# Kernel tuning notes

Hardware: AMD Instinct MI355X
Metric: run time of the kernel (lower is better)

The kernel has to match this reference:

```python
import jax, jax.numpy as jnp
import numpy as np

N = 128000      # total nodes
B = 128         # graphs, 1000 nodes each
L = 4           # max_levels
S_MAX = 1000    # max cluster size (<= PositionalEncoding max_len)
H = 128         # hidden dim (all conv output dims equal)
IN_DIM = 128
OUT_DIM = 1
E = 1024000
TEMP = 0.1


def layer_norm(x, g, b, eps=1e-5):
    mu = jnp.mean(x, axis=-1, keepdims=True)
    v = jnp.mean((x - mu) ** 2, axis=-1, keepdims=True)
    return (x - mu) * jax.lax.rsqrt(v + eps) * g + b


def transformer_conv(x, src, dst, Wq, bq, Wk, bk, Wv, bv, Ws, bs):
    # PyG TransformerConv, heads=1: softmax over in-edges of each dst node
    q = x @ Wq + bq
    k = x @ Wk + bk
    v = x @ Wv + bv
    logits = jnp.sum(q[dst] * k[src], axis=-1) / jnp.sqrt(jnp.float32(q.shape[-1]))
    m = jax.ops.segment_max(logits, dst, num_segments=N)
    e = jnp.exp(logits - m[dst])
    s = jax.ops.segment_sum(e, dst, num_segments=N)
    alpha = e / s[dst]
    agg = jax.ops.segment_sum(alpha[:, None] * v[src], dst, num_segments=N)
    return agg + x @ Ws + bs  # root_weight skip connection


def pos_encoding(S, d):
    pos = jnp.arange(S, dtype=jnp.float32)[:, None]
    div = jnp.exp(jnp.arange(0, d, 2, dtype=jnp.float32) * (-jnp.log(10000.0) / d))
    pe = jnp.zeros((S, d), jnp.float32)
    pe = pe.at[:, 0::2].set(jnp.sin(pos * div))
    pe = pe.at[:, 1::2].set(jnp.cos(pos * div))
    return pe


def gru(xseq, Wih, Whh, bih, bhh):
    # xseq: [G, S, H] -> outputs [G, S, H]; torch GRU gate math
    G = xseq.shape[0]
    def step(h, x_t):
        gi = x_t @ Wih.T + bih
        gh = h @ Whh.T + bhh
        ir, iz, inn = jnp.split(gi, 3, axis=-1)
        hr, hz, hn = jnp.split(gh, 3, axis=-1)
        r = jax.nn.sigmoid(ir + hr)
        z = jax.nn.sigmoid(iz + hz)
        n = jnp.tanh(inn + r * hn)
        h_new = (1.0 - z) * n + z * h
        return h_new, h_new
    h0 = jnp.zeros((G, Whh.shape[1]), xseq.dtype)
    _, outs = jax.lax.scan(step, h0, jnp.swapaxes(xseq, 0, 1))
    return jnp.swapaxes(outs, 0, 1)


def _forward(x, tree_edge_index, call_sequences, batch,
             conv_Wq, conv_bq, conv_Wk, conv_bk, conv_Wv, conv_bv, conv_Ws, conv_bs,
             ln_g, ln_b, centers, proj_W, proj_b,
             gru_Wih, gru_Whh, gru_bih, gru_bhh, seqln_g, seqln_b,
             lin1_W, lin1_b, lin2_W, lin2_b):
    src, dst = tree_edge_index[0], tree_edge_index[1]
    h = x
    for i in range(3):  # conv1/bn1, conv2/bn2, conv4/bn4
        h = transformer_conv(h, src, dst, conv_Wq[i], conv_bq[i], conv_Wk[i],
                             conv_bk[i], conv_Wv[i], conv_bv[i], conv_Ws[i], conv_bs[i])
        h = jax.nn.relu(layer_norm(h, ln_g[i], ln_b[i]))

    # HierarchicalClassifier: cosine-sim soft assignment + center variance loss
    xn = h / jnp.maximum(jnp.linalg.norm(h, axis=-1, keepdims=True), 1e-8)
    cn = centers / jnp.maximum(jnp.linalg.norm(centers, axis=-1, keepdims=True), 1e-8)
    assign = jax.nn.softmax((xn @ cn.T) / TEMP, axis=-1)
    level_ids = jnp.argmax(assign, axis=1).astype(jnp.int32)
    iu0, iu1 = np.triu_indices(L, k=1)
    dvec = jnp.linalg.norm(centers[iu0] - centers[iu1], axis=-1)
    distance = -jnp.var(dvec, ddof=1)  # torch.var is unbiased

    # ragged gather + pad: group nodes by (graph, cluster), sort by call order
    G = B * L
    group = batch * L + level_ids                       # [N]
    order = jnp.argsort(group * N + call_sequences)     # sort by group, then call
    g_sorted = group[order]
    counts = jax.ops.segment_sum(jnp.ones((N,), jnp.int32), group, num_segments=G)
    starts = jnp.cumsum(counts) - counts
    pos = jnp.arange(N, dtype=jnp.int32) - starts[g_sorted]
    seq = jnp.zeros((G, S_MAX, H), h.dtype).at[g_sorted, pos].set(h[order])

    # SequentialRNN: proj -> pos-enc -> GRU -> LayerNorm -> ReLU (mask unused)
    sin = seq @ proj_W + proj_b + pos_encoding(S_MAX, H)[None]
    outs = gru(sin, gru_Wih, gru_Whh, gru_bih, gru_bhh)
    outs = jax.nn.relu(layer_norm(outs, seqln_g, seqln_b))

    # scatter valid positions back; singleton clusters keep raw features
    node_out = jnp.zeros_like(h).at[order].set(outs[g_sorted, pos])
    singleton = (counts[group] == 1)
    gout = jnp.where(singleton[:, None], h, node_out)

    y = jax.nn.gelu(gout @ lin1_W + lin1_b, approximate=False)
    y = jax.nn.sigmoid(y @ lin2_W + lin2_b)
    return y, distance


def setup_inputs():
    key = jax.random.key(0)
    ks = jax.random.split(key, 16)
    p = lambda k, s: jax.random.normal(k, s, jnp.float32) * 0.02
    return {
        "x": jax.random.normal(ks[0], (N, IN_DIM), jnp.float32),
        "tree_edge_index": jax.random.randint(ks[1], (2, E), 0, N, dtype=jnp.int32),
        "call_sequences": jax.random.permutation(ks[2], N).astype(jnp.int32),
        "batch": (jnp.arange(N, dtype=jnp.int32) * B) // N,  # 1000 nodes per graph
        "conv_Wq": p(ks[3], (3, H, H)), "conv_bq": jnp.zeros((3, H), jnp.float32),
        "conv_Wk": p(ks[4], (3, H, H)), "conv_bk": jnp.zeros((3, H), jnp.float32),
        "conv_Wv": p(ks[5], (3, H, H)), "conv_bv": jnp.zeros((3, H), jnp.float32),
        "conv_Ws": p(ks[6], (3, H, H)), "conv_bs": jnp.zeros((3, H), jnp.float32),
        "ln_g": jnp.ones((3, H), jnp.float32), "ln_b": jnp.zeros((3, H), jnp.float32),
        "centers": jax.random.normal(ks[7], (L, H), jnp.float32),
        "proj_W": p(ks[8], (H, H)), "proj_b": jnp.zeros((H,), jnp.float32),
        "gru_Wih": p(ks[9], (3 * H, H)), "gru_Whh": p(ks[10], (3 * H, H)),
        "gru_bih": jnp.zeros((3 * H,), jnp.float32), "gru_bhh": jnp.zeros((3 * H,), jnp.float32),
        "seqln_g": jnp.ones((H,), jnp.float32), "seqln_b": jnp.zeros((H,), jnp.float32),
        "lin1_W": p(ks[11], (H, 8)), "lin1_b": jnp.zeros((8,), jnp.float32),
        "lin2_W": p(ks[12], (8, OUT_DIM)), "lin2_b": jnp.zeros((OUT_DIM,), jnp.float32),
    }


def reference(x, tree_edge_index, call_sequences, batch,
              conv_Wq, conv_bq, conv_Wk, conv_bk, conv_Wv, conv_bv, conv_Ws, conv_bs,
              ln_g, ln_b, centers, proj_W, proj_b,
              gru_Wih, gru_Whh, gru_bih, gru_bhh, seqln_g, seqln_b,
              lin1_W, lin1_b, lin2_W, lin2_b):
    return _forward(x, tree_edge_index, call_sequences, batch,
                    conv_Wq, conv_bq, conv_Wk, conv_bk, conv_Wv, conv_bv, conv_Ws, conv_bs,
                    ln_g, ln_b, centers, proj_W, proj_b,
                    gru_Wih, gru_Whh, gru_bih, gru_bhh, seqln_g, seqln_b,
                    lin1_W, lin1_b, lin2_W, lin2_b)
```

## Files before the change

### kernel.cpp

```cpp
#include <hip/hip_runtime.h>

#define NN 128000
#define EE 1024000
#define HH 128
#define GG 512
#define SMAX 1000
#define NCHUNK 500

typedef unsigned int u32;
typedef unsigned short u16;

constexpr size_t NH     = (size_t)NN*HH;
constexpr size_t F_H    = 0;
constexpr size_t F_A    = NH;
constexpr size_t F_B    = 2*NH;
constexpr size_t F_NODE = F_A + (size_t)NN*192;
constexpr size_t F_QB   = 3*NH;
constexpr size_t F_CN   = F_QB  + NN;
constexpr size_t F_WKT  = F_CN  + 512;
constexpr size_t F_CW   = F_WKT + 3*16384;
constexpr size_t F_PEW  = F_CW  + 128*384;
constexpr size_t F_PEB  = F_PEW + 1000*384;
constexpr size_t F_END  = F_PEB + 1000*128;

constexpr size_t I_ROWP = 0;
constexpr size_t I_CUR  = I_ROWP + NN + 8;
constexpr size_t I_COL  = I_CUR  + NN;
constexpr size_t I_GRP  = I_COL  + EE;
constexpr size_t I_INV  = I_GRP  + NN;
constexpr size_t I_POS  = I_INV  + NN;
constexpr size_t I_GN   = I_POS  + NN;
constexpr size_t I_CNT  = I_GN   + (size_t)GG*SMAX;
constexpr size_t I_CH   = I_CNT  + GG;
constexpr size_t I_BS   = I_CH   + (size_t)NCHUNK*GG;
constexpr size_t I_WT   = I_BS   + 512;
constexpr size_t I_END  = I_WT   + 64*384;

constexpr size_t WS_NEEDED = F_END*4 + I_END*4;

__device__ inline float wredf(float v){
  #pragma unroll
  for (int o = 32; o; o >>= 1) v += __shfl_xor(v, o);
  return v;
}
__device__ inline u32 bf16rne(float f){
  u32 u = __float_as_uint(f);
  return (u + 0x7fffu + ((u >> 16) & 1u)) >> 16;
}
__device__ inline float bf2f(u16 u){
  return __uint_as_float(((u32)u) << 16);
}
__device__ inline float frcp(float x){
#if __has_builtin(__builtin_amdgcn_rcpf)
  return __builtin_amdgcn_rcpf(x);
#else
  return 1.f / x;
#endif
}

typedef _Float16 h2_t __attribute__((ext_vector_type(2)));
__device__ inline float dot2f(u32 w, u32 h, float acc){
#if __has_builtin(__builtin_amdgcn_fdot2)
  return __builtin_amdgcn_fdot2(__builtin_bit_cast(h2_t, w),
                                __builtin_bit_cast(h2_t, h), acc, false);
#else
  float r;
  asm("v_dot2_f32_f16 %0, %1, %2, %3" : "=v"(r) : "v"(w), "v"(h), "v"(acc));
  return r;
#endif
}
#define PIN4(v) asm volatile("" : "+v"((v).x), "+v"((v).y), "+v"((v).z), "+v"((v).w))

__global__ void k_sentinel(float* __restrict__ out, int n, float val){
  int i = blockIdx.x * 256 + threadIdx.x;
  if (i < n) out[i] = val;
}

__global__ void k_zero(int* __restrict__ p){
  p[blockIdx.x * 256 + threadIdx.x] = 0;
}
__global__ void k_hist(const int* __restrict__ dst, int* __restrict__ deg){
  int e = blockIdx.x * 256 + threadIdx.x;
  atomicAdd(&deg[dst[e]], 1);
}
__global__ void k_s1(const int* __restrict__ deg, int* __restrict__ bsum){
  __shared__ int red[256];
  int t = threadIdx.x;
  red[t] = deg[blockIdx.x * 256 + t];
  __syncthreads();
  for (int s = 128; s; s >>= 1){ if (t < s) red[t] += red[t + s]; __syncthreads(); }
  if (!t) bsum[blockIdx.x] = red[0];
}
__global__ void k_s2(int* __restrict__ bsum){
  __shared__ int arr[512];
  int t = threadIdx.x;
  int v0 = (t < NCHUNK) ? bsum[t] : 0;
  arr[t] = v0; __syncthreads();
  for (int off = 1; off < 512; off <<= 1){
    int v = (t >= off) ? arr[t - off] : 0;
    __syncthreads();
    arr[t] += v;
    __syncthreads();
  }
  if (t < NCHUNK) bsum[t] = arr[t] - v0;
}
__global__ void k_s3(const int* __restrict__ bsum, int* __restrict__ row_ptr,
                     int* __restrict__ cursor){
  __shared__ int arr[256];
  int t = threadIdx.x;
  int i = blockIdx.x * 256 + t;
  int v0 = cursor[i];
  arr[t] = v0; __syncthreads();
  for (int off = 1; off < 256; off <<= 1){
    int v = (t >= off) ? arr[t - off] : 0;
    __syncthreads();
    arr[t] += v;
    __syncthreads();
  }
  int exc = arr[t] - v0 + bsum[blockIdx.x];
  row_ptr[i] = exc;
  cursor[i]  = exc;
  if (i == 0) row_ptr[NN] = EE;
}
__global__ void k_scatter(const int* __restrict__ src, const int* __restrict__ dst,
                          int* __restrict__ cursor, int* __restrict__ col){
  int e = blockIdx.x * 256 + threadIdx.x;
  int idx = atomicAdd(&cursor[dst[e]], 1);
  col[idx] = src[e];
}

__global__ void k_setup(const float* __restrict__ centers, float* __restrict__ cn,
                        float* __restrict__ dist_out){
  __shared__ float red[128];
  int t = threadIdx.x;
  for (int l = 0; l < 4; ++l){
    float v = centers[l*128 + t];
    red[t] = v * v; __syncthreads();
    for (int s = 64; s; s >>= 1){ if (t < s) red[t] += red[t + s]; __syncthreads(); }
    float nrm = sqrtf(red[0]);
    __syncthreads();
    cn[l*128 + t] = v / fmaxf(nrm, 1e-8f);
  }
  const int iu0[6] = {0,0,0,1,1,2}, iu1[6] = {1,2,3,2,3,3};
  __shared__ float dv[6];
  for (int p = 0; p < 6; ++p){
    float d = centers[iu0[p]*128 + t] - centers[iu1[p]*128 + t];
    red[t] = d * d; __syncthreads();
    for (int s = 64; s; s >>= 1){ if (t < s) red[t] += red[t + s]; __syncthreads(); }
    if (!t) dv[p] = sqrtf(red[0]);
    __syncthreads();
  }
  if (!t){
    float mean = 0.f;
    for (int p = 0; p < 6; ++p) mean += dv[p];
    mean /= 6.f;
    float var = 0.f;
    for (int p = 0; p < 6; ++p){ float d = dv[p] - mean; var += d * d; }
    var /= 5.f;
    dist_out[0] = -var;
  }
}

__global__ void k_pe(const float* __restrict__ projb, float* __restrict__ peb){
  int p = blockIdx.x, t = threadIdx.x;
  float ex  = (float)(t >> 1) * (-2.0f * 9.210340371976184f / 128.0f);
  float ang = (float)p * expf(ex);
  float v = (t & 1) ? cosf(ang) : sinf(ang);
  peb[p*128 + t] = v + projb[t];
}
__global__ void k_pew(const float* __restrict__ peb, const float* __restrict__ Wih,
                      const float* __restrict__ bih, float* __restrict__ pew){
  int p = blockIdx.x;
  int j = blockIdx.y * 128 + threadIdx.x;
  const float* pb = peb + p*128;
  const float* wr = Wih + (size_t)j*128;
  float acc = bih[j];
  #pragma unroll 4
  for (int m = 0; m < 128; ++m) acc += pb[m] * wr[m];
  pew[(size_t)p*384 + j] = acc;
}
__global__ void k_combw(const float* __restrict__ projW, const float* __restrict__ Wih,
                        float* __restrict__ cw){
  int kk = blockIdx.x;
  int j  = blockIdx.y * 128 + threadIdx.x;
  const float* pr = projW + (size_t)kk*128;
  const float* wr = Wih + (size_t)j*128;
  float acc = 0.f;
  #pragma unroll 4
  for (int m = 0; m < 128; ++m) acc += pr[m] * wr[m];
  cw[(size_t)kk*384 + j] = acc;
}
__global__ void k_tr(const float* __restrict__ Wk, float* __restrict__ wkt){
  int kk = blockIdx.x, l = blockIdx.y, c = threadIdx.x;
  wkt[(size_t)l*16384 + kk*128 + c] = Wk[(size_t)l*16384 + c*128 + kk];
}
__global__ void k_packwhh16(const float* __restrict__ Whh, u32* __restrict__ wt){
  int kp = blockIdx.x;
  int j  = blockIdx.y * 128 + threadIdx.x;
  _Float16 a = (_Float16)Whh[(size_t)j*128 + 2*kp];
  _Float16 b = (_Float16)Whh[(size_t)j*128 + 2*kp + 1];
  u32 lo = (u32)__builtin_bit_cast(u16, a);
  u32 hi = (u32)__builtin_bit_cast(u16, b);
  wt[(size_t)j*64 + kp] = (hi << 16) | lo;
}

__global__ __launch_bounds__(256, 2) void k_gemm(
    const float* __restrict__ X, const float* __restrict__ W, int ldw,
    const float* __restrict__ X2, const float* __restrict__ W2,
    const float* __restrict__ bias, const float* __restrict__ pew,
    const int* __restrict__ pos, float* __restrict__ out,
    u16* __restrict__ outb, int ldo){
  __shared__ __align__(16) float Wl[64*132];
  __shared__ __align__(16) float Xl[64*132];
  int tid = threadIdx.x;
  int rb = blockIdx.x * 128;
  int cb = blockIdx.y * 128;
  int rg = tid >> 4;
  int cg = tid & 15;
  int kxor = (cg >> 2) & 3;
  float acc[8][8];
  #pragma unroll
  for (int a = 0; a < 8; ++a)
    #pragma unroll
    for (int b = 0; b < 8; ++b) acc[a][b] = 0.f;
  int nhalf = X2 ? 4 : 2;
  for (int half = 0; half < nhalf; ++half){
    const float* Xs = (half < 2) ? X : X2;
    const float* Ws = (half < 2) ? W : W2;
    int ldws = (half < 2) ? ldw : 128;
    int hk = half & 1;
    __syncthreads();
    #pragma unroll
    for (int it = 0; it < 8; ++it){
      int idx = it*256 + tid;
      int kk = idx >> 5, c4 = idx & 31;
      *(float4*)&Wl[kk*132 + c4*4] =
          *(const float4*)&Ws[(size_t)(hk*64 + kk)*ldws + cb + c4*4];
    }
    #pragma unroll
    for (int it = 0; it < 8; ++it){
      int idx = it*256 + tid;
      int r = idx >> 4, c4 = idx & 15;
      float4 xv = *(const float4*)&Xs[(size_t)(rb + r)*128 + hk*64 + c4*4];
      Xl[(c4*4+0)*132 + r] = xv.x;
      Xl[(c4*4+1)*132 + r] = xv.y;
      Xl[(c4*4+2)*132 + r] = xv.z;
      Xl[(c4*4+3)*132 + r] = xv.w;
    }
    __syncthreads();
    #pragma unroll 2
    for (int kk = 0; kk < 64; ++kk){
      int kx = kk ^ kxor;
      float4 wa = *(const float4*)&Wl[kx*132 + cg*8];
      float4 wb = *(const float4*)&Wl[kx*132 + cg*8 + 4];
      float4 xa = *(const float4*)&Xl[kx*132 + rg*8];
      float4 xb = *(const float4*)&Xl[kx*132 + rg*8 + 4];
      float xs[8] = {xa.x, xa.y, xa.z, xa.w, xb.x, xb.y, xb.z, xb.w};
      float ws[8] = {wa.x, wa.y, wa.z, wa.w, wb.x, wb.y, wb.z, wb.w};
      #pragma unroll
      for (int rr = 0; rr < 8; ++rr)
        #pragma unroll
        for (int j = 0; j < 8; ++j) acc[rr][j] += xs[rr] * ws[j];
    }
  }
  #pragma unroll
  for (int rr = 0; rr < 8; ++rr){
    int r = rb + rg*8 + rr;
    float bv[8];
    if (pos){
      const float* pw = pew + (size_t)pos[r]*384 + cb + cg*8;
      #pragma unroll
      for (int j = 0; j < 8; ++j) bv[j] = pw[j];
    } else if (bias){
      #pragma unroll
      for (int j = 0; j < 8; ++j) bv[j] = bias[cb + cg*8 + j];
    } else {
      #pragma unroll
      for (int j = 0; j < 8; ++j) bv[j] = 0.f;
    }
    if (outb){
      u16 ob[8];
      #pragma unroll
      for (int j = 0; j < 8; ++j) ob[j] = (u16)bf16rne(acc[rr][j] + bv[j]);
      *(uint4*)(outb + (size_t)r*ldo + cb + cg*8) = *(const uint4*)ob;
    } else {
      float ov[8];
      #pragma unroll
      for (int j = 0; j < 8; ++j) ov[j] = acc[rr][j] + bv[j];
      float* op = out + (size_t)r*ldo + cb + cg*8;
      *(float4*)op       = *(const float4*)&ov[0];
      *(float4*)(op + 4) = *(const float4*)&ov[4];
    }
  }
}

__global__ __launch_bounds__(256) void k_rowdot(
    const float* __restrict__ q, const float* __restrict__ bk,
    float* __restrict__ qb){
  int d = blockIdx.x * 4 + (threadIdx.x >> 6);
  int lane = threadIdx.x & 63;
  float2 qv = *(const float2*)&q[(size_t)d*128 + 2*lane];
  float2 bv = *(const float2*)&bk[2*lane];
  float p = wredf(qv.x * bv.x + qv.y * bv.y);
  if (lane == 0) qb[d] = p;
}

__global__ __launch_bounds__(256) void k_edge(
    const float* __restrict__ qt, const float* __restrict__ qb,
    const float* __restrict__ xsrc, const int* __restrict__ row_ptr,
    const int* __restrict__ col, float* __restrict__ xagg){
  int d = blockIdx.x * 4 + (threadIdx.x >> 6);
  int lane = threadIdx.x & 63;
  int e0 = row_ptr[d], e1 = row_ptr[d+1];
  if (e0 == e1){
    *(float2*)&xagg[(size_t)d*128 + 2*lane] = make_float2(0.f, 0.f);
    return;
  }
  float2 qv = *(const float2*)&qt[(size_t)d*128 + 2*lane];
  float qbd = qb[d];
  float ssum = 0.f, a0 = 0.f, a1 = 0.f;
  for (int e = e0; e < e1; ++e){
    int s = col[e];
    float2 xv = *(const float2*)&xsrc[(size_t)s*128 + 2*lane];
    float p = wredf(qv.x * xv.x + qv.y * xv.y);
    float el = __expf((p + qbd) * 0.08838834764831845f);
    ssum += el;
    a0 += el * xv.x;
    a1 += el * xv.y;
  }
  float inv = 1.f / ssum;
  *(float2*)&xagg[(size_t)d*128 + 2*lane] = make_float2(a0 * inv, a1 * inv);
}

__global__ __launch_bounds__(256) void k_lnrelu(
    const float* __restrict__ in, const float* __restrict__ g,
    const float* __restrict__ b, const float* __restrict__ bvv,
    const int* __restrict__ rowp, float* __restrict__ outp){
  int node = blockIdx.x * 4 + (threadIdx.x >> 6);
  int lane = threadIdx.x & 63;
  float x0 = in[(size_t)node*128 + 2*lane], x1 = in[(size_t)node*128 + 2*lane + 1];
  if (bvv && rowp[node+1] > rowp[node]){
    x0 += bvv[2*lane];
    x1 += bvv[2*lane + 1];
  }
  float s = wredf(x0 + x1);
  float qq = wredf(x0*x0 + x1*x1);
  float mu = s * 0.0078125f;
  float var = qq * 0.0078125f - mu*mu;
  float rstd = rsqrtf(var + 1e-5f);
  float y0 = (x0 - mu)*rstd*g[2*lane]   + b[2*lane];
  float y1 = (x1 - mu)*rstd*g[2*lane+1] + b[2*lane+1];
  outp[(size_t)node*128 + 2*lane]     = fmaxf(y0, 0.f);
  outp[(size_t)node*128 + 2*lane + 1] = fmaxf(y1, 0.f);
}

__global__ __launch_bounds__(256) void k_postln(
    u16* __restrict__ no, const float* __restrict__ g, const float* __restrict__ b){
  int node = blockIdx.x * 4 + (threadIdx.x >> 6);
  int lane = threadIdx.x & 63;
  float x0 = bf2f(no[(size_t)node*128 + 2*lane]);
  float x1 = bf2f(no[(size_t)node*128 + 2*lane + 1]);
  float s = wredf(x0 + x1);
  float qq = wredf(x0*x0 + x1*x1);
  float mu = s * 0.0078125f;
  float var = qq * 0.0078125f - mu*mu;
  float rstd = rsqrtf(var + 1e-5f);
  float y0 = (x0 - mu)*rstd*g[2*lane]   + b[2*lane];
  float y1 = (x1 - mu)*rstd*g[2*lane+1] + b[2*lane+1];
  no[(size_t)node*128 + 2*lane]     = (u16)bf16rne(fmaxf(y0, 0.f));
  no[(size_t)node*128 + 2*lane + 1] = (u16)bf16rne(fmaxf(y1, 0.f));
}

__global__ __launch_bounds__(256) void k_classify(
    const float* __restrict__ h, const float* __restrict__ cn,
    const int* __restrict__ batch, const int* __restrict__ callsq,
    int* __restrict__ grp, int* __restrict__ inv){
  int node = blockIdx.x * 4 + (threadIdx.x >> 6);
  int lane = threadIdx.x & 63;
  float h0 = h[(size_t)node*128 + 2*lane], h1 = h[(size_t)node*128 + 2*lane + 1];
  float p0 = h0*cn[      2*lane] + h1*cn[      2*lane+1];
  float p1 = h0*cn[128 + 2*lane] + h1*cn[128 + 2*lane+1];
  float p2 = h0*cn[256 + 2*lane] + h1*cn[256 + 2*lane+1];
  float p3 = h0*cn[384 + 2*lane] + h1*cn[384 + 2*lane+1];
  p0 = wredf(p0); p1 = wredf(p1); p2 = wredf(p2); p3 = wredf(p3);
  if (lane == 0){
    float best = p0; int bi = 0;
    if (p1 > best){ best = p1; bi = 1; }
    if (p2 > best){ best = p2; bi = 2; }
    if (p3 > best){ best = p3; bi = 3; }
    grp[node] = batch[node]*4 + bi;
    inv[callsq[node]] = node;
  }
}

__global__ __launch_bounds__(256) void k_g1(const int* __restrict__ inv,
                                            const int* __restrict__ grp,
                                            int* __restrict__ ch){
  __shared__ int hist[GG];
  int c = blockIdx.x, t = threadIdx.x;
  hist[t] = 0; hist[t + 256] = 0;
  __syncthreads();
  int g = grp[inv[c*256 + t]];
  atomicAdd(&hist[g], 1);
  __syncthreads();
  ch[c*GG + t] = hist[t];
  ch[c*GG + 256 + t] = hist[256 + t];
}
__global__ void k_g2(int* __restrict__ ch, int* __restrict__ cnt){
  __shared__ int arr[512];
  int g = blockIdx.x, t = threadIdx.x;
  int v0 = (t < NCHUNK) ? ch[(size_t)t*GG + g] : 0;
  arr[t] = v0; __syncthreads();
  for (int off = 1; off < 512; off <<= 1){
    int v = (t >= off) ? arr[t - off] : 0;
    __syncthreads();
    arr[t] += v;
    __syncthreads();
  }
  if (t < NCHUNK) ch[(size_t)t*GG + g] = arr[t] - v0;
  if (t == 511) cnt[g] = arr[511];
}
__global__ __launch_bounds__(256) void k_g3(
    const int* __restrict__ inv, const int* __restrict__ grp,
    const int* __restrict__ ch, int* __restrict__ pos, int* __restrict__ gn){
  __shared__ int hist[GG];
  int c = blockIdx.x, t = threadIdx.x;
  hist[t] = 0; hist[t + 256] = 0;
  __syncthreads();
  int node = inv[c*256 + t];
  int g = grp[node];
  int lane = t & 63, w = t >> 6;
  int before = 0, total = 0;
  for (int j = 0; j < 64; ++j){
    int gj = __shfl(g, j);
    if (gj == g){ total++; if (j < lane) before++; }
  }
  int base = 0;
  for (int wv = 0; wv < 4; ++wv){
    if (w == wv){
      base = hist[g];
      if (before == total - 1) hist[g] = base + total;
    }
    __syncthreads();
  }
  int p = ch[c*GG + g] + base + before;
  pos[node] = p;
  gn[(size_t)g*SMAX + p] = node;
}

__global__ __launch_bounds__(256)
__attribute__((amdgpu_waves_per_eu(2, 2)))
void k_gru(
    const u16* __restrict__ gi, const u32* __restrict__ wt,
    const float* __restrict__ bhh, const int* __restrict__ gn,
    const int* __restrict__ cnt, u16* __restrict__ node_out){
  __shared__ __align__(16) u16 hb16[2][128];
  int t = threadIdx.x;
  int j = t >> 1;
  int kh = t & 1;
  int g = blockIdx.x;
  int my = cnt[g];
  if (my <= 1) return;
  uint4 wr_[8], wz_[8], wn_[8];
  {
    const uint4* wt4 = (const uint4*)wt;
    size_t b0 = (size_t)(0*128 + j)*16 + kh*8;
    size_t b1 = (size_t)(1*128 + j)*16 + kh*8;
    size_t b2 = (size_t)(2*128 + j)*16 + kh*8;
    #pragma unroll
    for (int s = 0; s < 8; ++s){
      wr_[s] = wt4[b0 + s];
      wz_[s] = wt4[b1 + s];
      wn_[s] = wt4[b2 + s];
    }
    #pragma unroll
    for (int s = 0; s < 8; ++s){
      PIN4(wr_[s]); PIN4(wz_[s]); PIN4(wn_[s]);
    }
  }
  if (t < 128) hb16[0][t] = 0;
  float br = bhh[j], bz = bhh[128 + j], bn = bhh[256 + j];
  const int* gnr = gn + (size_t)g*SMAX;
  float hprev = 0.f;
  int nA = gnr[0];
  int nB = gnr[min(1, my - 1)];
  int nC = gnr[min(2, my - 1)];
  const u16* gA = gi + (size_t)nA*384;
  const u16* gB = gi + (size_t)nB*384;
  const u16* gC = gi + (size_t)nC*384;
  float axr = bf2f(gA[j]), axz = bf2f(gA[128 + j]), axn = bf2f(gA[256 + j]);
  float bxr = bf2f(gB[j]), bxz = bf2f(gB[128 + j]), bxn = bf2f(gB[256 + j]);
  float cxr = bf2f(gC[j]), cxz = bf2f(gC[128 + j]), cxn = bf2f(gC[256 + j]);
  __syncthreads();
  for (int p = 0; p < my; ++p){
    int cur = p & 1, nxt = cur ^ 1;
    float xr = axr, xz = axz, xn = axn;
    int node = nA;
    axr = bxr; axz = bxz; axn = bxn; nA = nB;
    bxr = cxr; bxz = cxz; bxn = cxn; nB = nC;
    nC = gnr[min(p + 3, my - 1)];
    const u16* gN = gi + (size_t)nC*384;
    cxr = bf2f(gN[j]); cxz = bf2f(gN[128 + j]); cxn = bf2f(gN[256 + j]);
    const uint4* HB = (const uint4*)&hb16[cur][0];
    uint4 hh[8];
    #pragma unroll
    for (int s = 0; s < 8; ++s) hh[s] = HB[kh*8 + s];
    float ar = 0.f, az = 0.f, an = 0.f;
    #pragma unroll
    for (int s = 0; s < 8; ++s){
      ar = dot2f(wr_[s].x, hh[s].x, ar); az = dot2f(wz_[s].x, hh[s].x, az); an = dot2f(wn_[s].x, hh[s].x, an);
      ar = dot2f(wr_[s].y, hh[s].y, ar); az = dot2f(wz_[s].y, hh[s].y, az); an = dot2f(wn_[s].y, hh[s].y, an);
      ar = dot2f(wr_[s].z, hh[s].z, ar); az = dot2f(wz_[s].z, hh[s].z, az); an = dot2f(wn_[s].z, hh[s].z, an);
      ar = dot2f(wr_[s].w, hh[s].w, ar); az = dot2f(wz_[s].w, hh[s].w, az); an = dot2f(wn_[s].w, hh[s].w, an);
    }
    ar += __shfl_xor(ar, 1); az += __shfl_xor(az, 1); an += __shfl_xor(an, 1);
    ar += br; az += bz; an += bn;
    float er = __expf(-(xr + ar));
    float r  = frcp(1.f + er);
    float ez = __expf(-(xz + az));
    float z  = frcp(1.f + ez);
    float y  = xn + r * an;
    float e2 = __expf(-2.f * y);
    float n  = (1.f - e2) * frcp(1.f + e2);
    float hnew = n + z * (hprev - n);
    hprev = hnew;
    if (!kh){
      _Float16 hf = (_Float16)hnew;
      hb16[nxt][j] = __builtin_bit_cast(u16, hf);
      node_out[(size_t)node*128 + j] = (u16)bf16rne(hnew);
    }
    __syncthreads();
  }
}

__global__ __launch_bounds__(256) void k_head(
    const float* __restrict__ h, const u16* __restrict__ node_out,
    const int* __restrict__ grp, const int* __restrict__ cnt,
    const float* __restrict__ l1W, const float* __restrict__ l1b,
    const float* __restrict__ l2W, const float* __restrict__ l2b,
    float* __restrict__ out){
  int node = blockIdx.x * 4 + (threadIdx.x >> 6);
  int lane = threadIdx.x & 63;
  bool single = (cnt[grp[node]] == 1);
  float x0, x1;
  if (single){
    x0 = h[(size_t)node*128 + 2*lane];
    x1 = h[(size_t)node*128 + 2*lane + 1];
  } else {
    x0 = bf2f(node_out[(size_t)node*128 + 2*lane]);
    x1 = bf2f(node_out[(size_t)node*128 + 2*lane + 1]);
  }
  float acc[8];
  #pragma unroll
  for (int j = 0; j < 8; ++j)
    acc[j] = x0 * l1W[(2*lane)*8 + j] + x1 * l1W[(2*lane + 1)*8 + j];
  #pragma unroll
  for (int o = 32; o; o >>= 1)
    #pragma unroll
    for (int j = 0; j < 8; ++j) acc[j] += __shfl_xor(acc[j], o);
  if (lane == 0){
    float zz = l2b[0];
    #pragma unroll
    for (int j = 0; j < 8; ++j){
      float xx = acc[j] + l1b[j];
      float ge = 0.5f * xx * (1.f + erff(xx * 0.7071067811865476f));
      zz += ge * l2W[j];
    }
    out[node] = 1.f / (1.f + expf(-zz));
  }
}

extern "C" void kernel_launch(void* const* d_in, const int* in_sizes, int n_in,
                              void* d_out, int out_size, void* d_ws, size_t ws_size,
                              hipStream_t stream){
  float* out = (float*)d_out;

  if (ws_size < WS_NEEDED){
    float code = -(float)(ws_size >> 20);
    k_sentinel<<<(out_size + 255)/256, 256, 0, stream>>>(out, out_size, code);
    return;
  }

  const float* x       = (const float*)d_in[0];
  const int*   tei     = (const int*)d_in[1];
  const int*   callsq  = (const int*)d_in[2];
  const int*   batch   = (const int*)d_in[3];
  const float* Wq      = (const float*)d_in[4];
  const float* bq      = (const float*)d_in[5];
  const float* Wk      = (const float*)d_in[6];
  const float* bk      = (const float*)d_in[7];
  const float* Wv      = (const float*)d_in[8];
  const float* bv      = (const float*)d_in[9];
  const float* Wsk     = (const float*)d_in[10];
  const float* bsk     = (const float*)d_in[11];
  const float* lng     = (const float*)d_in[12];
  const float* lnb     = (const float*)d_in[13];
  const float* centers = (const float*)d_in[14];
  const float* projW   = (const float*)d_in[15];
  const float* projb   = (const float*)d_in[16];
  const float* Wih     = (const float*)d_in[17];
  const float* Whh     = (const float*)d_in[18];
  const float* bih     = (const float*)d_in[19];
  const float* bhh     = (const float*)d_in[20];
  const float* sqg     = (const float*)d_in[21];
  const float* sqb     = (const float*)d_in[22];
  const float* l1W     = (const float*)d_in[23];
  const float* l1b     = (const float*)d_in[24];
  const float* l2W     = (const float*)d_in[25];
  const float* l2b     = (const float*)d_in[26];

  float* wf = (float*)d_ws;
  float* f_h    = wf + F_H;
  float* f_a    = wf + F_A;
  float* f_b    = wf + F_B;
  float* f_qb   = wf + F_QB;
  float* f_cn   = wf + F_CN;
  float* f_wkt  = wf + F_WKT;
  float* f_cw   = wf + F_CW;
  float* f_pew  = wf + F_PEW;
  float* f_peb  = wf + F_PEB;
  u16*   gi_bf  = (u16*)(wf + F_A);
  u16*   no_bf  = (u16*)(wf + F_NODE);
  int* wi = (int*)(wf + F_END);
  int* i_rowp = wi + I_ROWP;
  int* i_cur  = wi + I_CUR;
  int* i_col  = wi + I_COL;
  int* i_grp  = wi + I_GRP;
  int* i_inv  = wi + I_INV;
  int* i_pos  = wi + I_POS;
  int* i_gn   = wi + I_GN;
  int* i_cnt  = wi + I_CNT;
  int* i_ch   = wi + I_CH;
  int* i_bs   = wi + I_BS;
  u32* i_wt   = (u32*)(wi + I_WT);

  const int* esrc = tei;
  const int* edst = tei + EE;

  k_zero<<<NN/256, 256, 0, stream>>>(i_cur);
  k_hist<<<EE/256, 256, 0, stream>>>(edst, i_cur);
  k_s1<<<NCHUNK, 256, 0, stream>>>(i_cur, i_bs);
  k_s2<<<1, 512, 0, stream>>>(i_bs);
  k_s3<<<NCHUNK, 256, 0, stream>>>(i_bs, i_rowp, i_cur);
  k_scatter<<<EE/256, 256, 0, stream>>>(esrc, edst, i_cur, i_col);

  k_setup<<<1, 128, 0, stream>>>(centers, f_cn, out + NN);
  k_pe<<<1000, 128, 0, stream>>>(projb, f_peb);
  k_pew<<<dim3(1000, 3), 128, 0, stream>>>(f_peb, Wih, bih, f_pew);
  k_tr<<<dim3(128, 3), 128, 0, stream>>>(Wk, f_wkt);
  k_combw<<<dim3(128, 3), 128, 0, stream>>>(projW, Wih, f_cw);
  k_packwhh16<<<dim3(64, 3), 128, 0, stream>>>(Whh, i_wt);

  for (int i = 0; i < 3; ++i){
    const float* xin = i ? f_h : x;
    size_t wo = (size_t)i * 128 * 128, bo = (size_t)i * 128;
    k_gemm<<<dim3(NN/128, 1), 256, 0, stream>>>(xin, Wq + wo, 128, nullptr, nullptr,
        bq + bo, nullptr, nullptr, f_a, nullptr, 128);
    k_rowdot<<<NN/4, 256, 0, stream>>>(f_a, bk + bo, f_qb);
    k_gemm<<<dim3(NN/128, 1), 256, 0, stream>>>(f_a, f_wkt + (size_t)i*16384, 128,
        nullptr, nullptr, nullptr, nullptr, nullptr, f_b, nullptr, 128);
    k_edge<<<NN/4, 256, 0, stream>>>(f_b, f_qb, xin, i_rowp, i_col, f_a);
    k_gemm<<<dim3(NN/128, 1), 256, 0, stream>>>(f_a, Wv + wo, 128, xin, Wsk + wo,
        bsk + bo, nullptr, nullptr, f_b, nullptr, 128);
    k_lnrelu<<<NN/4, 256, 0, stream>>>(f_b, lng + bo, lnb + bo, bv + bo, i_rowp, f_h);
  }

  k_classify<<<NN/4, 256, 0, stream>>>(f_h, f_cn, batch, callsq, i_grp, i_inv);
  k_g1<<<NCHUNK, 256, 0, stream>>>(i_inv, i_grp, i_ch);
  k_g2<<<GG, 512, 0, stream>>>(i_ch, i_cnt);
  k_g3<<<NCHUNK, 256, 0, stream>>>(i_inv, i_grp, i_ch, i_pos, i_gn);

  k_gemm<<<dim3(NN/128, 3), 256, 0, stream>>>(f_h, f_cw, 384, nullptr, nullptr,
      nullptr, f_pew, i_pos, nullptr, gi_bf, 384);

  k_gru<<<GG, 256, 0, stream>>>(gi_bf, i_wt, bhh, i_gn, i_cnt, no_bf);
  k_postln<<<NN/4, 256, 0, stream>>>(no_bf, sqg, sqb);

  k_head<<<NN/4, 256, 0, stream>>>(f_h, no_bf, i_grp, i_cnt, l1W, l1b, l2W, l2b, out);
}
```

Before: 2.569 ms.

## Fold Wq·WkT into one GEMM, fuse LN with classify and head, retune edge kernel

Precomputes Wq·Wk^T along with the bias-derived vectors and scalar. Each layer then runs one node GEMM instead of two, and the q·bk row dot is computed directly from x. The edge kernel now uses 32 lanes per node with float4 loads and prefetches the next source row. The last-layer LayerNorm is fused with clustering classification, and the sequence LayerNorm is folded into the head kernel, removing two elementwise passes. A setprio hint is added to the GRU inner loop. Risks are slight numeric drift from the reassociated matmul and a different edge-parallel shape.

```diff
diff --git a/kernel.cpp b/kernel.cpp
--- a/kernel.cpp
+++ b/kernel.cpp
@@ -16,12 +16,16 @@
 constexpr size_t F_B    = 2*NH;
 constexpr size_t F_NODE = F_A + (size_t)NN*192;
 constexpr size_t F_QB   = 3*NH;
-constexpr size_t F_CN   = F_QB  + NN;
-constexpr size_t F_WKT  = F_CN  + 512;
-constexpr size_t F_CW   = F_WKT + 3*16384;
-constexpr size_t F_PEW  = F_CW  + 128*384;
-constexpr size_t F_PEB  = F_PEW + 1000*384;
-constexpr size_t F_END  = F_PEB + 1000*128;
+constexpr size_t F_CN   = F_QB   + NN;
+constexpr size_t F_WKT  = F_CN   + 512;
+constexpr size_t F_WQK  = F_WKT  + 3*16384;
+constexpr size_t F_BQK  = F_WQK  + 3*16384;
+constexpr size_t F_WQBK = F_BQK  + 3*128;
+constexpr size_t F_QBB  = F_WQBK + 3*128;
+constexpr size_t F_CW   = F_QBB  + 8;
+constexpr size_t F_PEW  = F_CW   + 128*384;
+constexpr size_t F_PEB  = F_PEW  + 1000*384;
+constexpr size_t F_END  = F_PEB  + 1000*128;
 
 constexpr size_t I_ROWP = 0;
 constexpr size_t I_CUR  = I_ROWP + NN + 8;
@@ -193,6 +197,25 @@
 __global__ void k_tr(const float* __restrict__ Wk, float* __restrict__ wkt){
   int kk = blockIdx.x, l = blockIdx.y, c = threadIdx.x;
   wkt[(size_t)l*16384 + kk*128 + c] = Wk[(size_t)l*16384 + c*128 + kk];
+}
+__global__ void k_mv(const float* __restrict__ M, const float* __restrict__ v,
+                     float* __restrict__ out){
+  int l = blockIdx.x, i = threadIdx.x;
+  const float* row = M + (size_t)l*16384 + (size_t)i*128;
+  const float* vv = v + l*128;
+  float acc = 0.f;
+  #pragma unroll 4
+  for (int j = 0; j < 128; ++j) acc += row[j] * vv[j];
+  out[l*128 + i] = acc;
+}
+__global__ void k_bb(const float* __restrict__ bq, const float* __restrict__ bk,
+                     float* __restrict__ qbb){
+  __shared__ float red[128];
+  int l = blockIdx.x, t = threadIdx.x;
+  red[t] = bq[l*128 + t] * bk[l*128 + t];
+  __syncthreads();
+  for (int s = 64; s; s >>= 1){ if (t < s) red[t] += red[t + s]; __syncthreads(); }
+  if (!t) qbb[l] = red[0];
 }
 __global__ void k_packwhh16(const float* __restrict__ Whh, u32* __restrict__ wt){
   int kp = blockIdx.x;
@@ -295,41 +318,46 @@
 }
 
 __global__ __launch_bounds__(256) void k_rowdot(
-    const float* __restrict__ q, const float* __restrict__ bk,
-    float* __restrict__ qb){
+    const float* __restrict__ x, const float* __restrict__ w,
+    const float* __restrict__ scal, float* __restrict__ qb){
   int d = blockIdx.x * 4 + (threadIdx.x >> 6);
   int lane = threadIdx.x & 63;
-  float2 qv = *(const float2*)&q[(size_t)d*128 + 2*lane];
-  float2 bv = *(const float2*)&bk[2*lane];
-  float p = wredf(qv.x * bv.x + qv.y * bv.y);
-  if (lane == 0) qb[d] = p;
+  float2 xv = *(const float2*)&x[(size_t)d*128 + 2*lane];
+  float2 wv = *(const float2*)&w[2*lane];
+  float p = wredf(xv.x * wv.x + xv.y * wv.y);
+  if (lane == 0) qb[d] = p + scal[0];
 }
 
 __global__ __launch_bounds__(256) void k_edge(
     const float* __restrict__ qt, const float* __restrict__ qb,
     const float* __restrict__ xsrc, const int* __restrict__ row_ptr,
     const int* __restrict__ col, float* __restrict__ xagg){
-  int d = blockIdx.x * 4 + (threadIdx.x >> 6);
-  int lane = threadIdx.x & 63;
+  int d = blockIdx.x * 8 + (threadIdx.x >> 5);
+  int lane = threadIdx.x & 31;
   int e0 = row_ptr[d], e1 = row_ptr[d+1];
   if (e0 == e1){
-    *(float2*)&xagg[(size_t)d*128 + 2*lane] = make_float2(0.f, 0.f);
+    *(float4*)&xagg[(size_t)d*128 + lane*4] = make_float4(0.f, 0.f, 0.f, 0.f);
     return;
   }
-  float2 qv = *(const float2*)&qt[(size_t)d*128 + 2*lane];
+  float4 qv = *(const float4*)&qt[(size_t)d*128 + lane*4];
   float qbd = qb[d];
-  float ssum = 0.f, a0 = 0.f, a1 = 0.f;
+  float ssum = 0.f, a0 = 0.f, a1 = 0.f, a2 = 0.f, a3 = 0.f;
+  float4 xc = *(const float4*)&xsrc[(size_t)col[e0]*128 + lane*4];
   for (int e = e0; e < e1; ++e){
-    int s = col[e];
-    float2 xv = *(const float2*)&xsrc[(size_t)s*128 + 2*lane];
-    float p = wredf(qv.x * xv.x + qv.y * xv.y);
+    float4 xn = xc;
+    if (e + 1 < e1)
+      xn = *(const float4*)&xsrc[(size_t)col[e+1]*128 + lane*4];
+    float p = qv.x*xc.x + qv.y*xc.y + qv.z*xc.z + qv.w*xc.w;
+    #pragma unroll
+    for (int o = 16; o; o >>= 1) p += __shfl_xor(p, o);
     float el = __expf((p + qbd) * 0.08838834764831845f);
     ssum += el;
-    a0 += el * xv.x;
-    a1 += el * xv.y;
+    a0 += el * xc.x; a1 += el * xc.y; a2 += el * xc.z; a3 += el * xc.w;
+    xc = xn;
   }
   float inv = 1.f / ssum;
-  *(float2*)&xagg[(size_t)d*128 + 2*lane] = make_float2(a0 * inv, a1 * inv);
+  *(float4*)&xagg[(size_t)d*128 + lane*4] =
+      make_float4(a0*inv, a1*inv, a2*inv, a3*inv);
 }
 
 __global__ __launch_bounds__(256) void k_lnrelu(
@@ -354,34 +382,32 @@
   outp[(size_t)node*128 + 2*lane + 1] = fmaxf(y1, 0.f);
 }
 
-__global__ __launch_bounds__(256) void k_postln(
-    u16* __restrict__ no, const float* __restrict__ g, const float* __restrict__ b){
+__global__ __launch_bounds__(256) void k_lnrelu_cls(
+    const float* __restrict__ in, const float* __restrict__ g,
+    const float* __restrict__ b, const float* __restrict__ bvv,
+    const int* __restrict__ rowp, float* __restrict__ outp,
+    const float* __restrict__ cn, const int* __restrict__ batch,
+    const int* __restrict__ callsq, int* __restrict__ grp, int* __restrict__ inv){
   int node = blockIdx.x * 4 + (threadIdx.x >> 6);
   int lane = threadIdx.x & 63;
-  float x0 = bf2f(no[(size_t)node*128 + 2*lane]);
-  float x1 = bf2f(no[(size_t)node*128 + 2*lane + 1]);
+  float x0 = in[(size_t)node*128 + 2*lane], x1 = in[(size_t)node*128 + 2*lane + 1];
+  if (rowp[node+1] > rowp[node]){
+    x0 += bvv[2*lane];
+    x1 += bvv[2*lane + 1];
+  }
   float s = wredf(x0 + x1);
   float qq = wredf(x0*x0 + x1*x1);
   float mu = s * 0.0078125f;
   float var = qq * 0.0078125f - mu*mu;
   float rstd = rsqrtf(var + 1e-5f);
-  float y0 = (x0 - mu)*rstd*g[2*lane]   + b[2*lane];
-  float y1 = (x1 - mu)*rstd*g[2*lane+1] + b[2*lane+1];
-  no[(size_t)node*128 + 2*lane]     = (u16)bf16rne(fmaxf(y0, 0.f));
-  no[(size_t)node*128 + 2*lane + 1] = (u16)bf16rne(fmaxf(y1, 0.f));
-}
-
-__global__ __launch_bounds__(256) void k_classify(
-    const float* __restrict__ h, const float* __restrict__ cn,
-    const int* __restrict__ batch, const int* __restrict__ callsq,
-    int* __restrict__ grp, int* __restrict__ inv){
-  int node = blockIdx.x * 4 + (threadIdx.x >> 6);
-  int lane = threadIdx.x & 63;
-  float h0 = h[(size_t)node*128 + 2*lane], h1 = h[(size_t)node*128 + 2*lane + 1];
-  float p0 = h0*cn[      2*lane] + h1*cn[      2*lane+1];
-  float p1 = h0*cn[128 + 2*lane] + h1*cn[128 + 2*lane+1];
-  float p2 = h0*cn[256 + 2*lane] + h1*cn[256 + 2*lane+1];
-  float p3 = h0*cn[384 + 2*lane] + h1*cn[384 + 2*lane+1];
+  float y0 = fmaxf((x0 - mu)*rstd*g[2*lane]   + b[2*lane],   0.f);
+  float y1 = fmaxf((x1 - mu)*rstd*g[2*lane+1] + b[2*lane+1], 0.f);
+  outp[(size_t)node*128 + 2*lane]     = y0;
+  outp[(size_t)node*128 + 2*lane + 1] = y1;
+  float p0 = y0*cn[      2*lane] + y1*cn[      2*lane+1];
+  float p1 = y0*cn[128 + 2*lane] + y1*cn[128 + 2*lane+1];
+  float p2 = y0*cn[256 + 2*lane] + y1*cn[256 + 2*lane+1];
+  float p3 = y0*cn[384 + 2*lane] + y1*cn[384 + 2*lane+1];
   p0 = wredf(p0); p1 = wredf(p1); p2 = wredf(p2); p3 = wredf(p3);
   if (lane == 0){
     float best = p0; int bi = 0;
@@ -505,6 +531,7 @@
     uint4 hh[8];
     #pragma unroll
     for (int s = 0; s < 8; ++s) hh[s] = HB[kh*8 + s];
+    __builtin_amdgcn_s_setprio(1);
     float ar = 0.f, az = 0.f, an = 0.f;
     #pragma unroll
     for (int s = 0; s < 8; ++s){
@@ -523,6 +550,7 @@
     float e2 = __expf(-2.f * y);
     float n  = (1.f - e2) * frcp(1.f + e2);
     float hnew = n + z * (hprev - n);
+    __builtin_amdgcn_s_setprio(0);
     hprev = hnew;
     if (!kh){
       _Float16 hf = (_Float16)hnew;
@@ -536,6 +564,7 @@
 __global__ __launch_bounds__(256) void k_head(
     const float* __restrict__ h, const u16* __restrict__ node_out,
     const int* __restrict__ grp, const int* __restrict__ cnt,
+    const float* __restrict__ sqg, const float* __restrict__ sqb,
     const float* __restrict__ l1W, const float* __restrict__ l1b,
     const float* __restrict__ l2W, const float* __restrict__ l2b,
     float* __restrict__ out){
@@ -547,8 +576,15 @@
     x0 = h[(size_t)node*128 + 2*lane];
     x1 = h[(size_t)node*128 + 2*lane + 1];
   } else {
-    x0 = bf2f(node_out[(size_t)node*128 + 2*lane]);
-    x1 = bf2f(node_out[(size_t)node*128 + 2*lane + 1]);
+    float r0 = bf2f(node_out[(size_t)node*128 + 2*lane]);
+    float r1 = bf2f(node_out[(size_t)node*128 + 2*lane + 1]);
+    float s = wredf(r0 + r1);
+    float qq = wredf(r0*r0 + r1*r1);
+    float mu = s * 0.0078125f;
+    float var = qq * 0.0078125f - mu*mu;
+    float rstd = rsqrtf(var + 1e-5f);
+    x0 = fmaxf((r0 - mu)*rstd*sqg[2*lane]   + sqb[2*lane],   0.f);
+    x1 = fmaxf((r1 - mu)*rstd*sqg[2*lane+1] + sqb[2*lane+1], 0.f);
   }
   float acc[8];
   #pragma unroll
@@ -616,6 +652,10 @@
   float* f_qb   = wf + F_QB;
   float* f_cn   = wf + F_CN;
   float* f_wkt  = wf + F_WKT;
+  float* f_wqk  = wf + F_WQK;
+  float* f_bqk  = wf + F_BQK;
+  float* f_wqbk = wf + F_WQBK;
+  float* f_qbb  = wf + F_QBB;
   float* f_cw   = wf + F_CW;
   float* f_pew  = wf + F_PEW;
   float* f_peb  = wf + F_PEB;
@@ -648,24 +688,32 @@
   k_pe<<<1000, 128, 0, stream>>>(projb, f_peb);
   k_pew<<<dim3(1000, 3), 128, 0, stream>>>(f_peb, Wih, bih, f_pew);
   k_tr<<<dim3(128, 3), 128, 0, stream>>>(Wk, f_wkt);
+  for (int i = 0; i < 3; ++i)
+    k_gemm<<<dim3(1, 1), 256, 0, stream>>>(Wq + (size_t)i*16384, f_wkt + (size_t)i*16384,
+        128, nullptr, nullptr, nullptr, nullptr, nullptr, f_wqk + (size_t)i*16384,
+        nullptr, 128);
+  k_mv<<<3, 128, 0, stream>>>(Wq, bk, f_wqbk);
+  k_mv<<<3, 128, 0, stream>>>(Wk, bq, f_bqk);
+  k_bb<<<3, 128, 0, stream>>>(bq, bk, f_qbb);
   k_combw<<<dim3(128, 3), 128, 0, stream>>>(projW, Wih, f_cw);
   k_packwhh16<<<dim3(64, 3), 128, 0, stream>>>(Whh, i_wt);
 
   for (int i = 0; i < 3; ++i){
     const float* xin = i ? f_h : x;
     size_t wo = (size_t)i * 128 * 128, bo = (size_t)i * 128;
-    k_gemm<<<dim3(NN/128, 1), 256, 0, stream>>>(xin, Wq + wo, 128, nullptr, nullptr,
-        bq + bo, nullptr, nullptr, f_a, nullptr, 128);
-    k_rowdot<<<NN/4, 256, 0, stream>>>(f_a, bk + bo, f_qb);
-    k_gemm<<<dim3(NN/128, 1), 256, 0, stream>>>(f_a, f_wkt + (size_t)i*16384, 128,
-        nullptr, nullptr, nullptr, nullptr, nullptr, f_b, nullptr, 128);
-    k_edge<<<NN/4, 256, 0, stream>>>(f_b, f_qb, xin, i_rowp, i_col, f_a);
+    k_gemm<<<dim3(NN/128, 1), 256, 0, stream>>>(xin, f_wqk + (size_t)i*16384, 128,
+        nullptr, nullptr, f_bqk + bo, nullptr, nullptr, f_b, nullptr, 128);
+    k_rowdot<<<NN/4, 256, 0, stream>>>(xin, f_wqbk + bo, f_qbb + i, f_qb);
+    k_edge<<<NN/8, 256, 0, stream>>>(f_b, f_qb, xin, i_rowp, i_col, f_a);
     k_gemm<<<dim3(NN/128, 1), 256, 0, stream>>>(f_a, Wv + wo, 128, xin, Wsk + wo,
         bsk + bo, nullptr, nullptr, f_b, nullptr, 128);
-    k_lnrelu<<<NN/4, 256, 0, stream>>>(f_b, lng + bo, lnb + bo, bv + bo, i_rowp, f_h);
-  }
-
-  k_classify<<<NN/4, 256, 0, stream>>>(f_h, f_cn, batch, callsq, i_grp, i_inv);
+    if (i < 2)
+      k_lnrelu<<<NN/4, 256, 0, stream>>>(f_b, lng + bo, lnb + bo, bv + bo, i_rowp, f_h);
+    else
+      k_lnrelu_cls<<<NN/4, 256, 0, stream>>>(f_b, lng + bo, lnb + bo, bv + bo, i_rowp,
+          f_h, f_cn, batch, callsq, i_grp, i_inv);
+  }
+
   k_g1<<<NCHUNK, 256, 0, stream>>>(i_inv, i_grp, i_ch);
   k_g2<<<GG, 512, 0, stream>>>(i_ch, i_cnt);
   k_g3<<<NCHUNK, 256, 0, stream>>>(i_inv, i_grp, i_ch, i_pos, i_gn);
@@ -674,7 +722,7 @@
       nullptr, f_pew, i_pos, nullptr, gi_bf, 384);
 
   k_gru<<<GG, 256, 0, stream>>>(gi_bf, i_wt, bhh, i_gn, i_cnt, no_bf);
-  k_postln<<<NN/4, 256, 0, stream>>>(no_bf, sqg, sqb);
-
-  k_head<<<NN/4, 256, 0, stream>>>(f_h, no_bf, i_grp, i_cnt, l1W, l1b, l2W, l2b, out);
-}
+
+  k_head<<<NN/4, 256, 0, stream>>>(f_h, no_bf, i_grp, i_cnt, sqg, sqb,
+                                   l1W, l1b, l2W, l2b, out);
+}
```

Result: faster. 2.258 ms (-12.1%).
